# Kernel optimization log

Hardware: AMD Instinct MI355X
Metric: run time of the kernel (lower is better)

The kernel has to match this reference:

```python
import jax, jax.numpy as jnp
import numpy as np

# Constant from livnium.kernel.constants (assumed scalar; value taken as 1.0).
K_O = 1.0
EPS = 1e-12  # F.normalize default eps

B, D, C = 16384, 1024, 3
F_DIM = D + 10  # features = h_final (D) + 10 scalar features


def setup_inputs() -> dict:
    key = jax.random.key(0)
    ks = jax.random.split(key, 8)
    s1 = 1.0 / np.sqrt(F_DIM)
    return {
        "h_final": jax.random.normal(ks[0], (B, D), jnp.float32),
        "v_p": jax.random.normal(ks[1], (B, D), jnp.float32),
        "v_h": jax.random.normal(ks[2], (B, D), jnp.float32),
        "neutral_dir": jax.random.normal(ks[3], (D,), jnp.float32),
        "neutral_scale": jnp.array(1.0, jnp.float32),
        "w1": jax.random.normal(ks[4], (F_DIM, F_DIM), jnp.float32) * s1,
        "b1": jnp.zeros((F_DIM,), jnp.float32),
        "w2": jax.random.normal(ks[5], (C, F_DIM), jnp.float32) * s1,
        "b2": jnp.zeros((C,), jnp.float32),
    }


def _normalize(x, axis):
    n = jnp.linalg.norm(x, axis=axis, keepdims=True)
    return x / jnp.maximum(n, EPS)


def reference(h_final, v_p, v_h, neutral_dir, neutral_scale, w1, b1, w2, b2):
    v_p_n = _normalize(v_p, -1)                      # [B, D]
    v_h_n = _normalize(v_h, -1)                      # [B, D]
    nd_n = _normalize(neutral_dir, 0)                # [D]

    # alignment(): cosine of the unit vectors == batched dot product.
    align = jnp.sum(v_p_n * v_h_n, axis=-1, keepdims=True)        # [B, 1]
    opp = jnp.sum(-v_p_n * v_h_n, axis=-1, keepdims=True)          # [B, 1]
    align_neutral_p = neutral_scale * jnp.sum(v_p_n * nd_n, axis=-1, keepdims=True)
    align_neutral_h = neutral_scale * jnp.sum(v_h_n * nd_n, axis=-1, keepdims=True)

    energy = K_O * ((1.0 + align) * 0.5)
    expose_neg = (1.0 - align) * 0.5
    dist_p_h = jnp.linalg.norm(v_h - v_p, axis=-1, keepdims=True)
    r_p = jnp.linalg.norm(v_p, axis=-1, keepdims=True)
    r_h = jnp.linalg.norm(v_h, axis=-1, keepdims=True)
    r_final = jnp.linalg.norm(h_final, axis=-1, keepdims=True)

    features = jnp.concatenate(
        [h_final, align, opp, energy, expose_neg, dist_p_h,
         r_p, r_h, r_final, align_neutral_p, align_neutral_h], axis=-1)  # [B, D+10]

    hidden = jax.nn.relu(features @ w1.T + b1)
    logits = hidden @ w2.T + b2                      # [B, C]
    return logits
```

## Files before the change

kernel.cpp:

```cpp
#include <hip/hip_runtime.h>
#include <cstdint>
#include <cstddef>

#define B_ROWS 16384
#define D_DIM  1024
#define F_REAL 1034
#define N_PAD  1152
#define K_PAD  1088
#define NK     (K_PAD / 64)
#define EPSN   1e-12f

typedef __bf16 bf16x8 __attribute__((ext_vector_type(8)));
typedef float  f32x4  __attribute__((ext_vector_type(4)));
typedef unsigned short u16;

__device__ __forceinline__ u16 f2bf(float f) {
    __bf16 b = (__bf16)f;
    return __builtin_bit_cast(u16, b);
}

__global__ __launch_bounds__(256)
void prep_kernel(const float* __restrict__ h, const float* __restrict__ vp,
                 const float* __restrict__ vh, const float* __restrict__ nd,
                 const float* __restrict__ nsp, u16* __restrict__ A)
{
    const int tid  = threadIdx.x;
    const int lane = tid & 63;
    const int wg   = blockIdx.x * 4 + (tid >> 6);
    const int r0   = wg * 4;

    const float4* ndp = (const float4*)nd;
    float4 n[4];
    #pragma unroll
    for (int c = 0; c < 4; ++c) n[c] = ndp[lane + c * 64];
    const float ns = nsp[0];

    float s_nn = 0.f;
    #pragma unroll
    for (int c = 0; c < 4; ++c)
        s_nn += n[c].x*n[c].x + n[c].y*n[c].y + n[c].z*n[c].z + n[c].w*n[c].w;
    #pragma unroll
    for (int m = 32; m >= 1; m >>= 1) s_nn += __shfl_xor(s_nn, m, 64);
    const float nnc = fmaxf(sqrtf(s_nn), EPSN);

    float4 P[2][4], Q[2][4], F[2][4];

#define LOADR(st, r)                                                          \
    do {                                                                      \
        const float4* vpp = (const float4*)(vp + (size_t)(r) * D_DIM);        \
        const float4* vhp = (const float4*)(vh + (size_t)(r) * D_DIM);        \
        const float4* hp  = (const float4*)(h  + (size_t)(r) * D_DIM);        \
        _Pragma("unroll")                                                     \
        for (int c = 0; c < 4; ++c) P[st][c] = vpp[lane + c * 64];            \
        _Pragma("unroll")                                                     \
        for (int c = 0; c < 4; ++c) Q[st][c] = vhp[lane + c * 64];            \
        _Pragma("unroll")                                                     \
        for (int c = 0; c < 4; ++c) F[st][c] = hp[lane + c * 64];             \
    } while (0)

    LOADR(0, r0);
    #pragma unroll
    for (int i = 0; i < 4; ++i) {
        const int st = i & 1;
        if (i + 1 < 4) LOADR(((i + 1) & 1), r0 + i + 1);
        __builtin_amdgcn_sched_barrier(0);

        float s_pp = 0.f, s_hh = 0.f, s_pv = 0.f, s_ff = 0.f;
        float s_dd = 0.f, s_pn = 0.f, s_hn = 0.f;
        #pragma unroll
        for (int c = 0; c < 4; ++c) {
            float4 p = P[st][c], q = Q[st][c], f = F[st][c], nn = n[c];
            s_pp += p.x*p.x + p.y*p.y + p.z*p.z + p.w*p.w;
            s_hh += q.x*q.x + q.y*q.y + q.z*q.z + q.w*q.w;
            s_pv += p.x*q.x + p.y*q.y + p.z*q.z + p.w*q.w;
            s_ff += f.x*f.x + f.y*f.y + f.z*f.z + f.w*f.w;
            float dx = q.x-p.x, dy = q.y-p.y, dz = q.z-p.z, dw = q.w-p.w;
            s_dd += dx*dx + dy*dy + dz*dz + dw*dw;
            s_pn += p.x*nn.x + p.y*nn.y + p.z*nn.z + p.w*nn.w;
            s_hn += q.x*nn.x + q.y*nn.y + q.z*nn.z + q.w*nn.w;
        }

        u16* arow = A + (size_t)(r0 + i) * K_PAD;
        #pragma unroll
        for (int c = 0; c < 4; ++c) {
            ushort4 hc;
            hc.x = f2bf(F[st][c].x); hc.y = f2bf(F[st][c].y);
            hc.z = f2bf(F[st][c].z); hc.w = f2bf(F[st][c].w);
            *(ushort4*)(arow + (lane + c * 64) * 4) = hc;
        }

        #pragma unroll
        for (int m = 32; m >= 1; m >>= 1) {
            s_pp += __shfl_xor(s_pp, m, 64);
            s_hh += __shfl_xor(s_hh, m, 64);
            s_pv += __shfl_xor(s_pv, m, 64);
            s_ff += __shfl_xor(s_ff, m, 64);
            s_dd += __shfl_xor(s_dd, m, 64);
            s_pn += __shfl_xor(s_pn, m, 64);
            s_hn += __shfl_xor(s_hn, m, 64);
        }

        if (lane == 0) {
            float np_ = sqrtf(s_pp), nh_ = sqrtf(s_hh), nf = sqrtf(s_ff);
            float npc = fmaxf(np_, EPSN), nhc = fmaxf(nh_, EPSN);
            float align = s_pv / (npc * nhc);
            u16 fo[64];
            fo[0] = f2bf(align);
            fo[1] = f2bf(-align);
            fo[2] = f2bf(0.5f * (1.0f + align));
            fo[3] = f2bf(0.5f * (1.0f - align));
            fo[4] = f2bf(sqrtf(s_dd));
            fo[5] = f2bf(np_);
            fo[6] = f2bf(nh_);
            fo[7] = f2bf(nf);
            fo[8] = f2bf(ns * s_pn / (npc * nnc));
            fo[9] = f2bf(ns * s_hn / (nhc * nnc));
            #pragma unroll
            for (int k = 10; k < 64; ++k) fo[k] = 0;
            #pragma unroll
            for (int k = 0; k < 8; ++k)
                *(uint4*)(arow + D_DIM + k * 8) = *(uint4*)(fo + k * 8);
        }
    }
#undef LOADR
}

__global__ __launch_bounds__(256)
void convw_kernel(const float* __restrict__ w1, u16* __restrict__ Bm,
                  const float* __restrict__ b2, float* __restrict__ out)
{
    const int i = blockIdx.x;
    for (int j = threadIdx.x; j < K_PAD; j += 256) {
        float v = (i < F_REAL && j < F_REAL) ? w1[(size_t)i * F_REAL + j] : 0.0f;
        Bm[(size_t)i * K_PAD + j] = f2bf(v);
    }
    if (i < 192) {
        int o = i * 256 + threadIdx.x;
        out[o] = b2[o % 3];
    }
}

__global__ __launch_bounds__(256)
void gemm_kernel(const u16* __restrict__ A,
                 const u16* __restrict__ Bm,
                 const float* __restrict__ b1, const float* __restrict__ w2,
                 float* __restrict__ out)
{
    __shared__ __bf16 As[2 * 64 * 32];
    __shared__ __bf16 Bs[2 * 128 * 32];

    const int tid  = threadIdx.x;
    const int lane = tid & 63;
    const int wave = tid >> 6;
    const int wm = wave >> 1, wn = wave & 1;
    const int bm = blockIdx.x, bn = blockIdx.y;

    const u16* gaA;
    __bf16*    lA;
    {
        int row = tid >> 2;
        int kc  = (tid & 3) ^ ((tid >> 3) & 3);
        gaA = A + (size_t)(bm * 64 + row) * K_PAD + kc * 8;
        lA  = As + tid * 8;
    }
    const u16* gaB[2];
    __bf16*    lB[2];
    #pragma unroll
    for (int o = 0; o < 2; ++o) {
        int s   = o * 256 + tid;
        int row = s >> 2;
        int kc  = (s & 3) ^ ((s >> 3) & 3);
        gaB[o] = Bm + (size_t)(bn * 128 + row) * K_PAD + kc * 8;
        lB[o]  = Bs + s * 8;
    }

    const int col  = lane & 15;
    const int quad = lane >> 4;
    const int swz  = quad ^ ((col >> 1) & 3);
    int aoff[2], boff[4];
    #pragma unroll
    for (int i = 0; i < 2; ++i)
        aoff[i] = ((wm * 32 + i * 16 + col) * 4 + swz) * 8;
    #pragma unroll
    for (int j = 0; j < 4; ++j)
        boff[j] = ((wn * 64 + j * 16 + col) * 4 + swz) * 8;

    f32x4 acc[2][4];
    #pragma unroll
    for (int i = 0; i < 2; ++i)
        #pragma unroll
        for (int j = 0; j < 4; ++j)
            acc[i][j] = (f32x4){0.f, 0.f, 0.f, 0.f};

    uint4 a0_0, a1_0, b00_0, b01_0, b10_0, b11_0;
    uint4 a0_1, a1_1, b00_1, b01_1, b10_1, b11_1;

#define LOAD_STAGE(st, ko)                                                    \
    do {                                                                      \
        a0_##st  = *(const uint4*)(gaA + (ko));                               \
        a1_##st  = *(const uint4*)(gaA + (ko) + 32);                          \
        b00_##st = *(const uint4*)(gaB[0] + (ko));                            \
        b01_##st = *(const uint4*)(gaB[0] + (ko) + 32);                       \
        b10_##st = *(const uint4*)(gaB[1] + (ko));                            \
        b11_##st = *(const uint4*)(gaB[1] + (ko) + 32);                       \
    } while (0)

#define WRITE_STAGE(st)                                                       \
    do {                                                                      \
        *(uint4*)(lA)           = a0_##st;                                    \
        *(uint4*)(lA + 2048)    = a1_##st;                                    \
        *(uint4*)(lB[0])        = b00_##st;                                   \
        *(uint4*)(lB[0] + 4096) = b01_##st;                                   \
        *(uint4*)(lB[1])        = b10_##st;                                   \
        *(uint4*)(lB[1] + 4096) = b11_##st;                                   \
    } while (0)

#define COMPUTE_TILE                                                          \
    do {                                                                      \
        _Pragma("unroll")                                                     \
        for (int h = 0; h < 2; ++h) {                                         \
            const __bf16* Ab = As + h * 2048;                                 \
            const __bf16* Bb = Bs + h * 4096;                                 \
            bf16x8 av[2], bv[4];                                              \
            _Pragma("unroll")                                                 \
            for (int i = 0; i < 2; ++i) av[i] = *(const bf16x8*)(Ab + aoff[i]); \
            _Pragma("unroll")                                                 \
            for (int j = 0; j < 4; ++j) bv[j] = *(const bf16x8*)(Bb + boff[j]); \
            _Pragma("unroll")                                                 \
            for (int i = 0; i < 2; ++i)                                       \
                _Pragma("unroll")                                             \
                for (int j = 0; j < 4; ++j)                                   \
                    acc[i][j] = __builtin_amdgcn_mfma_f32_16x16x32_bf16(      \
                                    av[i], bv[j], acc[i][j], 0, 0, 0);        \
        }                                                                     \
    } while (0)

    LOAD_STAGE(0, 0);
    LOAD_STAGE(1, 64);
    WRITE_STAGE(0);
    __syncthreads();

    for (int kt = 0; kt < NK; kt += 2) {
        if (kt + 2 < NK) LOAD_STAGE(0, (kt + 2) * 64);
        COMPUTE_TILE;
        if (kt + 1 < NK) {
            __syncthreads();
            WRITE_STAGE(1);
            __syncthreads();

            if (kt + 3 < NK) LOAD_STAGE(1, (kt + 3) * 64);
            COMPUTE_TILE;
            if (kt + 2 < NK) {
                __syncthreads();
                WRITE_STAGE(0);
                __syncthreads();
            }
        }
    }

    float bias[4], w20[4], w21[4], w22[4];
    #pragma unroll
    for (int ni = 0; ni < 4; ++ni) {
        int n = bn * 128 + wn * 64 + ni * 16 + col;
        bool v = n < F_REAL;
        bias[ni] = v ? b1[n] : 0.0f;
        w20[ni]  = v ? w2[n] : 0.0f;
        w21[ni]  = v ? w2[F_REAL + n] : 0.0f;
        w22[ni]  = v ? w2[2 * F_REAL + n] : 0.0f;
    }
    #pragma unroll
    for (int mi = 0; mi < 2; ++mi) {
        float c0[4] = {0,0,0,0}, c1[4] = {0,0,0,0}, c2[4] = {0,0,0,0};
        #pragma unroll
        for (int ni = 0; ni < 4; ++ni) {
            #pragma unroll
            for (int r = 0; r < 4; ++r) {
                float hd = fmaxf(acc[mi][ni][r] + bias[ni], 0.0f);
                c0[r] += hd * w20[ni];
                c1[r] += hd * w21[ni];
                c2[r] += hd * w22[ni];
            }
        }
        #pragma unroll
        for (int m = 8; m >= 1; m >>= 1) {
            #pragma unroll
            for (int r = 0; r < 4; ++r) {
                c0[r] += __shfl_xor(c0[r], m, 64);
                c1[r] += __shfl_xor(c1[r], m, 64);
                c2[r] += __shfl_xor(c2[r], m, 64);
            }
        }
        if (col == 0) {
            int gm = bm * 64 + wm * 32 + mi * 16 + quad * 4;
            #pragma unroll
            for (int r = 0; r < 4; ++r) {
                atomicAdd(out + (size_t)(gm + r) * 3 + 0, c0[r]);
                atomicAdd(out + (size_t)(gm + r) * 3 + 1, c1[r]);
                atomicAdd(out + (size_t)(gm + r) * 3 + 2, c2[r]);
            }
        }
    }
#undef LOAD_STAGE
#undef WRITE_STAGE
#undef COMPUTE_TILE
}

extern "C" void kernel_launch(void* const* d_in, const int* in_sizes, int n_in,
                              void* d_out, int out_size, void* d_ws, size_t ws_size,
                              hipStream_t stream)
{
    const float* h  = (const float*)d_in[0];
    const float* vp = (const float*)d_in[1];
    const float* vh = (const float*)d_in[2];
    const float* nd = (const float*)d_in[3];
    const float* ns = (const float*)d_in[4];
    const float* w1 = (const float*)d_in[5];
    const float* b1 = (const float*)d_in[6];
    const float* w2 = (const float*)d_in[7];
    const float* b2 = (const float*)d_in[8];
    float* out = (float*)d_out;

    u16* Afull = (u16*)d_ws;
    u16* Bfull = Afull + (size_t)B_ROWS * K_PAD;

    prep_kernel<<<1024, 256, 0, stream>>>(h, vp, vh, nd, ns, Afull);
    convw_kernel<<<N_PAD, 256, 0, stream>>>(w1, Bfull, b2, out);
    gemm_kernel<<<dim3(B_ROWS / 64, N_PAD / 128), 256, 0, stream>>>(
        Afull, Bfull, b1, w2, out);
}
```

Baseline: 290.0 us.

## Fuse h_final bf16 conversion and norm into GEMM A-tile loads

```diff
diff --git a/kernel.cpp b/kernel.cpp
--- a/kernel.cpp
+++ b/kernel.cpp
@@ -13,16 +13,31 @@
 typedef __bf16 bf16x8 __attribute__((ext_vector_type(8)));
 typedef float  f32x4  __attribute__((ext_vector_type(4)));
 typedef unsigned short u16;
+typedef unsigned int   u32;
 
 __device__ __forceinline__ u16 f2bf(float f) {
     __bf16 b = (__bf16)f;
     return __builtin_bit_cast(u16, b);
 }
 
+__device__ __forceinline__ uint4 pack8(uint4 A, uint4 B, float& ssq) {
+    float f0 = __uint_as_float(A.x), f1 = __uint_as_float(A.y);
+    float f2 = __uint_as_float(A.z), f3 = __uint_as_float(A.w);
+    float f4 = __uint_as_float(B.x), f5 = __uint_as_float(B.y);
+    float f6 = __uint_as_float(B.z), f7 = __uint_as_float(B.w);
+    ssq += f0*f0 + f1*f1 + f2*f2 + f3*f3 + f4*f4 + f5*f5 + f6*f6 + f7*f7;
+    uint4 w;
+    w.x = (u32)f2bf(f0) | ((u32)f2bf(f1) << 16);
+    w.y = (u32)f2bf(f2) | ((u32)f2bf(f3) << 16);
+    w.z = (u32)f2bf(f4) | ((u32)f2bf(f5) << 16);
+    w.w = (u32)f2bf(f6) | ((u32)f2bf(f7) << 16);
+    return w;
+}
+
 __global__ __launch_bounds__(256)
-void prep_kernel(const float* __restrict__ h, const float* __restrict__ vp,
+void prep_kernel(const float* __restrict__ vp,
                  const float* __restrict__ vh, const float* __restrict__ nd,
-                 const float* __restrict__ nsp, u16* __restrict__ A)
+                 const float* __restrict__ nsp, u16* __restrict__ Ascal)
 {
     const int tid  = threadIdx.x;
     const int lane = tid & 63;
@@ -43,19 +58,16 @@
     for (int m = 32; m >= 1; m >>= 1) s_nn += __shfl_xor(s_nn, m, 64);
     const float nnc = fmaxf(sqrtf(s_nn), EPSN);
 
-    float4 P[2][4], Q[2][4], F[2][4];
+    float4 P[2][4], Q[2][4];
 
 #define LOADR(st, r)                                                          \
     do {                                                                      \
         const float4* vpp = (const float4*)(vp + (size_t)(r) * D_DIM);        \
         const float4* vhp = (const float4*)(vh + (size_t)(r) * D_DIM);        \
-        const float4* hp  = (const float4*)(h  + (size_t)(r) * D_DIM);        \
         _Pragma("unroll")                                                     \
         for (int c = 0; c < 4; ++c) P[st][c] = vpp[lane + c * 64];            \
         _Pragma("unroll")                                                     \
         for (int c = 0; c < 4; ++c) Q[st][c] = vhp[lane + c * 64];            \
-        _Pragma("unroll")                                                     \
-        for (int c = 0; c < 4; ++c) F[st][c] = hp[lane + c * 64];             \
     } while (0)
 
     LOADR(0, r0);
@@ -65,43 +77,32 @@
         if (i + 1 < 4) LOADR(((i + 1) & 1), r0 + i + 1);
         __builtin_amdgcn_sched_barrier(0);
 
-        float s_pp = 0.f, s_hh = 0.f, s_pv = 0.f, s_ff = 0.f;
+        float s_pp = 0.f, s_hh = 0.f, s_pv = 0.f;
         float s_dd = 0.f, s_pn = 0.f, s_hn = 0.f;
         #pragma unroll
         for (int c = 0; c < 4; ++c) {
-            float4 p = P[st][c], q = Q[st][c], f = F[st][c], nn = n[c];
+            float4 p = P[st][c], q = Q[st][c], nn = n[c];
             s_pp += p.x*p.x + p.y*p.y + p.z*p.z + p.w*p.w;
             s_hh += q.x*q.x + q.y*q.y + q.z*q.z + q.w*q.w;
             s_pv += p.x*q.x + p.y*q.y + p.z*q.z + p.w*q.w;
-            s_ff += f.x*f.x + f.y*f.y + f.z*f.z + f.w*f.w;
             float dx = q.x-p.x, dy = q.y-p.y, dz = q.z-p.z, dw = q.w-p.w;
             s_dd += dx*dx + dy*dy + dz*dz + dw*dw;
             s_pn += p.x*nn.x + p.y*nn.y + p.z*nn.z + p.w*nn.w;
             s_hn += q.x*nn.x + q.y*nn.y + q.z*nn.z + q.w*nn.w;
         }
 
-        u16* arow = A + (size_t)(r0 + i) * K_PAD;
-        #pragma unroll
-        for (int c = 0; c < 4; ++c) {
-            ushort4 hc;
-            hc.x = f2bf(F[st][c].x); hc.y = f2bf(F[st][c].y);
-            hc.z = f2bf(F[st][c].z); hc.w = f2bf(F[st][c].w);
-            *(ushort4*)(arow + (lane + c * 64) * 4) = hc;
-        }
-
         #pragma unroll
         for (int m = 32; m >= 1; m >>= 1) {
             s_pp += __shfl_xor(s_pp, m, 64);
             s_hh += __shfl_xor(s_hh, m, 64);
             s_pv += __shfl_xor(s_pv, m, 64);
-            s_ff += __shfl_xor(s_ff, m, 64);
             s_dd += __shfl_xor(s_dd, m, 64);
             s_pn += __shfl_xor(s_pn, m, 64);
             s_hn += __shfl_xor(s_hn, m, 64);
         }
 
         if (lane == 0) {
-            float np_ = sqrtf(s_pp), nh_ = sqrtf(s_hh), nf = sqrtf(s_ff);
+            float np_ = sqrtf(s_pp), nh_ = sqrtf(s_hh);
             float npc = fmaxf(np_, EPSN), nhc = fmaxf(nh_, EPSN);
             float align = s_pv / (npc * nhc);
             u16 fo[64];
@@ -112,14 +113,15 @@
             fo[4] = f2bf(sqrtf(s_dd));
             fo[5] = f2bf(np_);
             fo[6] = f2bf(nh_);
-            fo[7] = f2bf(nf);
+            fo[7] = 0;
             fo[8] = f2bf(ns * s_pn / (npc * nnc));
             fo[9] = f2bf(ns * s_hn / (nhc * nnc));
             #pragma unroll
             for (int k = 10; k < 64; ++k) fo[k] = 0;
+            u16* arow = Ascal + (size_t)(r0 + i) * 64;
             #pragma unroll
             for (int k = 0; k < 8; ++k)
-                *(uint4*)(arow + D_DIM + k * 8) = *(uint4*)(fo + k * 8);
+                *(uint4*)(arow + k * 8) = *(uint4*)(fo + k * 8);
         }
     }
 #undef LOADR
@@ -141,7 +143,8 @@
 }
 
 __global__ __launch_bounds__(256)
-void gemm_kernel(const u16* __restrict__ A,
+void gemm_kernel(const float* __restrict__ hsrc,
+                 const u16* __restrict__ Ascal,
                  const u16* __restrict__ Bm,
                  const float* __restrict__ b1, const float* __restrict__ w2,
                  float* __restrict__ out)
@@ -155,14 +158,12 @@
     const int wm = wave >> 1, wn = wave & 1;
     const int bm = blockIdx.x, bn = blockIdx.y;
 
-    const u16* gaA;
-    __bf16*    lA;
-    {
-        int row = tid >> 2;
-        int kc  = (tid & 3) ^ ((tid >> 3) & 3);
-        gaA = A + (size_t)(bm * 64 + row) * K_PAD + kc * 8;
-        lA  = As + tid * 8;
-    }
+    const int srow = tid >> 2;
+    const int achk = (tid & 3) ^ ((tid >> 3) & 3);
+    const float* gaH = hsrc  + (size_t)(bm * 64 + srow) * D_DIM + achk * 8;
+    const u16*   gaS = Ascal + (size_t)(bm * 64 + srow) * 64    + achk * 8;
+    __bf16* lA = As + tid * 8;
+
     const u16* gaB[2];
     __bf16*    lB[2];
     #pragma unroll
@@ -192,23 +193,42 @@
         for (int j = 0; j < 4; ++j)
             acc[i][j] = (f32x4){0.f, 0.f, 0.f, 0.f};
 
-    uint4 a0_0, a1_0, b00_0, b01_0, b10_0, b11_0;
-    uint4 a0_1, a1_1, b00_1, b01_1, b10_1, b11_1;
+    float ssq = 0.f;
+
+    uint4 a0_0, a1_0, a2_0, a3_0, b00_0, b01_0, b10_0, b11_0;
+    uint4 a0_1, a1_1, a2_1, a3_1, b00_1, b01_1, b10_1, b11_1;
 
 #define LOAD_STAGE(st, ko)                                                    \
     do {                                                                      \
-        a0_##st  = *(const uint4*)(gaA + (ko));                               \
-        a1_##st  = *(const uint4*)(gaA + (ko) + 32);                          \
+        if ((ko) == 1024) {                                                   \
+            a0_##st = *(const uint4*)(gaS);                                   \
+            a1_##st = *(const uint4*)(gaS + 32);                              \
+        } else {                                                              \
+            a0_##st = *(const uint4*)(gaH + (ko));                            \
+            a1_##st = *(const uint4*)(gaH + (ko) + 4);                        \
+            a2_##st = *(const uint4*)(gaH + (ko) + 32);                       \
+            a3_##st = *(const uint4*)(gaH + (ko) + 36);                       \
+        }                                                                     \
         b00_##st = *(const uint4*)(gaB[0] + (ko));                            \
         b01_##st = *(const uint4*)(gaB[0] + (ko) + 32);                       \
         b10_##st = *(const uint4*)(gaB[1] + (ko));                            \
         b11_##st = *(const uint4*)(gaB[1] + (ko) + 32);                       \
     } while (0)
 
-#define WRITE_STAGE(st)                                                       \
+#define WRITE_STAGE(st, scal)                                                 \
     do {                                                                      \
-        *(uint4*)(lA)           = a0_##st;                                    \
-        *(uint4*)(lA + 2048)    = a1_##st;                                    \
+        if (scal) {                                                           \
+            float s_ = ssq + __shfl_xor(ssq, 1, 64);                          \
+            s_ += __shfl_xor(s_, 2, 64);                                      \
+            u32 rb_ = (u32)f2bf(sqrtf(s_));                                   \
+            uint4 s0_ = a0_##st, s1_ = a1_##st;                               \
+            if (achk == 0) s0_.w = (s0_.w & 0xFFFFu) | (rb_ << 16);           \
+            *(uint4*)(lA)        = s0_;                                       \
+            *(uint4*)(lA + 2048) = s1_;                                       \
+        } else {                                                              \
+            *(uint4*)(lA)        = pack8(a0_##st, a1_##st, ssq);              \
+            *(uint4*)(lA + 2048) = pack8(a2_##st, a3_##st, ssq);              \
+        }                                                                     \
         *(uint4*)(lB[0])        = b00_##st;                                   \
         *(uint4*)(lB[0] + 4096) = b01_##st;                                   \
         *(uint4*)(lB[1])        = b10_##st;                                   \
@@ -237,7 +257,7 @@
 
     LOAD_STAGE(0, 0);
     LOAD_STAGE(1, 64);
-    WRITE_STAGE(0);
+    WRITE_STAGE(0, false);
     __syncthreads();
 
     for (int kt = 0; kt < NK; kt += 2) {
@@ -245,14 +265,14 @@
         COMPUTE_TILE;
         if (kt + 1 < NK) {
             __syncthreads();
-            WRITE_STAGE(1);
+            WRITE_STAGE(1, false);
             __syncthreads();
 
             if (kt + 3 < NK) LOAD_STAGE(1, (kt + 3) * 64);
             COMPUTE_TILE;
             if (kt + 2 < NK) {
                 __syncthreads();
-                WRITE_STAGE(0);
+                WRITE_STAGE(0, (kt + 2) == 16);
                 __syncthreads();
             }
         }
@@ -320,11 +340,11 @@
     const float* b2 = (const float*)d_in[8];
     float* out = (float*)d_out;
 
-    u16* Afull = (u16*)d_ws;
-    u16* Bfull = Afull + (size_t)B_ROWS * K_PAD;
-
-    prep_kernel<<<1024, 256, 0, stream>>>(h, vp, vh, nd, ns, Afull);
+    u16* Ascal = (u16*)d_ws;
+    u16* Bfull = Ascal + (size_t)B_ROWS * 64;
+
+    prep_kernel<<<1024, 256, 0, stream>>>(vp, vh, nd, ns, Ascal);
     convw_kernel<<<N_PAD, 256, 0, stream>>>(w1, Bfull, b2, out);
     gemm_kernel<<<dim3(B_ROWS / 64, N_PAD / 128), 256, 0, stream>>>(
-        Afull, Bfull, b1, w2, out);
-}
+        h, Ascal, Bfull, b1, w2, out);
+}
```

Measured after the change: 306.8 us. 1.06x slower.
